# Performance work log

Hardware: AMD Instinct MI355X
Metric: run time of the kernel (lower is better)

Reference implementation:

```python
import jax, jax.numpy as jnp
import numpy as np

K = 256  # top-k causal instances (init kwarg k)


def setup_inputs() -> dict:
    key = jax.random.key(0)
    k1, k2 = jax.random.split(key)
    B, N, D = 8, 4096, 128
    X = jax.random.normal(k1, (B, N, D), dtype=jnp.float32)
    W = jax.random.normal(k2, (1, D), dtype=jnp.float32) * (1.0 / np.sqrt(D))
    return {"X": X, "W": W}


def reference(X, W):
    B, N, D = X.shape
    # --- build_adjacency_matrix, batched over B ---
    Xc = X - X.mean(axis=1, keepdims=True)                       # center per feature
    cov = jnp.einsum('bnd,bmd->bnm', Xc, Xc)                     # [B,N,N]
    var = jnp.sqrt(jnp.sum(Xc * Xc, axis=-1, keepdims=True)) + 1e-6  # [B,N,1]
    A = jnp.abs(cov / (var * var.transpose(0, 2, 1)))            # |corr|, [B,N,N]
    d = jnp.sum(A, axis=-1) ** -0.5                              # [B,N]
    A_norm = d[:, :, None] * A * d[:, None, :]                   # D^{-1/2} A D^{-1/2}
    # --- GCN layer: A_norm @ (X @ W^T), squeeze to scores ---
    S = jnp.einsum('bnm,bm->bn', A_norm, (X @ W.T)[..., 0])      # [B,N]
    # --- topk split (torch.topk is sorted descending, as is lax.top_k) ---
    _, topk_idx = jax.lax.top_k(S, K)                            # [B,K]
    mask = jnp.ones((B, N), bool).at[jnp.arange(B)[:, None], topk_idx].set(False)
    # stable argsort of ~mask puts non-topk indices first, in ascending order
    non_idx = jnp.argsort(~mask, axis=1)[:, : N - K]             # [B,N-K]
    F_c = jnp.take_along_axis(X, topk_idx[:, :, None], axis=1)   # [B,K,D]
    F_nc = jnp.take_along_axis(X, non_idx[:, :, None], axis=1)   # [B,N-K,D]
    # NOTE: original code returns F_c (not the indices) as second output (bug preserved)
    return (S, F_c, F_c.mean(axis=1, keepdims=True), F_nc.mean(axis=1, keepdims=True))
```

## Files before the change

kernel.cpp:

```cpp
#include <hip/hip_runtime.h>


#define NN 4096
#define DD 128
#define KK 256
#define KT 128
#define NBLK 128
#define LDX 132

__device__ __forceinline__ float f4c(float4 v, int c) {
  return c == 0 ? v.x : c == 1 ? v.y : c == 2 ? v.z : v.w;
}

__global__ __launch_bounds__(128) void k_mean(
    const float* __restrict__ X, float* __restrict__ mean) {
#pragma clang fp contract(off)
  int b = blockIdx.x, d = threadIdx.x;
  const float* p = X + (size_t)b * NN * DD + d;
  float acc = 0.f;
#pragma unroll 32
  for (int n = 0; n < NN; ++n) acc = acc + p[(size_t)n * DD];
  mean[b * DD + d] = acc * (1.0f / 4096.0f);
}

__global__ __launch_bounds__(256) void k_rows(
    const float* __restrict__ X, const float* __restrict__ W,
    const float* __restrict__ mean, float* __restrict__ Xc,
    float* __restrict__ vvec, float* __restrict__ yvec) {
#pragma clang fp contract(off)
  __shared__ float wL[DD], mL[DD];
  int t = threadIdx.x;
  int b = blockIdx.x >> 4;
  if (t < DD) { wL[t] = W[t]; mL[t] = mean[b * DD + t]; }
  __syncthreads();
  int rg = blockIdx.x * 256 + t;
  const float* xp = X + (size_t)rg * DD;
  float* xcp = Xc + (size_t)rg * DD;
  float xc[DD];
  float x[DD];
#pragma unroll
  for (int i = 0; i < 32; ++i) {
    float4 v4 = *(const float4*)(xp + i * 4);
    x[i*4] = v4.x; x[i*4+1] = v4.y; x[i*4+2] = v4.z; x[i*4+3] = v4.w;
  }
#pragma unroll
  for (int d = 0; d < DD; ++d) xc[d] = x[d] - mL[d];
#pragma unroll
  for (int i = 0; i < 32; ++i) {
    float4 v4; v4.x = xc[i*4]; v4.y = xc[i*4+1]; v4.z = xc[i*4+2]; v4.w = xc[i*4+3];
    *(float4*)(xcp + i * 4) = v4;
  }
  float vs = 0.f;
#pragma unroll
  for (int d = 0; d < DD; ++d) {
    float p = xc[d] * xc[d];
    vs = vs + p;
  }
  vvec[rg] = sqrtf(vs) + 1e-6f;
  float ay[8] = {0.f,0.f,0.f,0.f,0.f,0.f,0.f,0.f};
#pragma unroll
  for (int d = 0; d < DD; ++d)
    ay[d & 7] = __builtin_fmaf(x[d], wL[d], ay[d & 7]);
  float e0 = ay[0] + ay[4], e1 = ay[1] + ay[5];
  float e2 = ay[2] + ay[6], e3 = ay[3] + ay[7];
  yvec[rg] = (e0 + e2) + (e1 + e3);
}

#define GRAM_PHASE(CUR, NXT, d0v, ncv, rbv)                                  \
  {                                                                          \
    const int nc_ = (ncv);                                                   \
    _Pragma("unroll")                                                        \
    for (int q = 0; q < 2; ++q)                                              \
      _Pragma("unroll")                                                      \
      for (int c = 0; c < 4; ++c)                                            \
        NXT[q][c] = *(const float4*)(xcrow[q] + nc_ * 16 + c * 4);           \
    const int d0_ = (d0v);                                                   \
    const int rb_ = (rbv);                                                   \
    _Pragma("unroll")                                                        \
    for (int k = 0; k < 8; ++k) {                                            \
      float4 m0 = *(const float4*)&Xm[rb_ + k * 8][d0_];                     \
      float4 m1 = *(const float4*)&Xm[rb_ + k * 8][d0_ + 4];                 \
      float4 m2 = *(const float4*)&Xm[rb_ + k * 8][d0_ + 8];                 \
      float4 m3 = *(const float4*)&Xm[rb_ + k * 8][d0_ + 12];                \
      _Pragma("unroll")                                                      \
      for (int dd = 0; dd < 16; ++dd) {                                      \
        float xmv = f4c(dd < 4 ? m0 : dd < 8 ? m1 : dd < 12 ? m2 : m3,       \
                        dd & 3);                                             \
        _Pragma("unroll")                                                    \
        for (int q = 0; q < 2; ++q)                                          \
          g[k][q] = __builtin_fmaf(f4c(CUR[q][dd >> 2], dd & 3), xmv,        \
                                   g[k][q]);                                 \
      }                                                                      \
    }                                                                        \
  }

template <int PASS>
__global__ __launch_bounds__(512, 1) void k_gram(
    const float* __restrict__ Xc, const float* __restrict__ vvec,
    const float* __restrict__ dvec, const float* __restrict__ yvec,
    float* __restrict__ outv) {
#pragma clang fp contract(off)
  __shared__ float Xm[KT][LDX];
  __shared__ float vmL[KT], dmL[KT], wmL[KT];
  __shared__ float red[NBLK][8];
  int bid = blockIdx.x;
  int b = bid & 7;
  int n0 = (bid >> 3) * NBLK;
  int t = threadIdx.x;
  int j = t & 7, nl = t >> 3;
  size_t base = (size_t)b * NN * DD;

  const float* xcrow[2];
  float vnq[2], dnq[2], acc[2];
#pragma unroll
  for (int q = 0; q < 2; ++q) {
    int n = n0 + nl * 2 + q;
    xcrow[q] = Xc + base + (size_t)n * DD;
    vnq[q] = vvec[b * NN + n];
    dnq[q] = (PASS == 1) ? dvec[b * NN + n] : 0.f;
    acc[q] = 0.f;
  }

  float4 xa[2][4], xb[2][4];
#pragma unroll
  for (int q = 0; q < 2; ++q)
#pragma unroll
    for (int c = 0; c < 4; ++c)
      xa[q][c] = *(const float4*)(xcrow[q] + c * 4);

  for (int mt = 0; mt < 32; ++mt) {
    __syncthreads();
#pragma unroll
    for (int i = 0; i < 8; ++i) {
      int e = t + i * 512;
      int r = e >> 5, c4 = e & 31;
      float4 v4 = *(const float4*)(Xc + base + (size_t)(mt * KT + r) * DD + c4 * 4);
      *(float4*)&Xm[r][c4 * 4] = v4;
    }
    if (t < KT) {
      vmL[t] = vvec[b * NN + mt * KT + t];
      if (PASS == 1) {
        dmL[t] = dvec[b * NN + mt * KT + t];
        wmL[t] = yvec[b * NN + mt * KT + t];
      }
    }
    __syncthreads();

    for (int kg = 0; kg < 2; ++kg) {
      float g[8][2];
#pragma unroll
      for (int k = 0; k < 8; ++k)
#pragma unroll
        for (int q = 0; q < 2; ++q) g[k][q] = 0.f;

      int rb = kg * 64 + j;
      for (int dc4 = 0; dc4 < 4; ++dc4) {
        GRAM_PHASE(xa, xb, dc4 * 32, 2 * dc4 + 1, rb);
        GRAM_PHASE(xb, xa, dc4 * 32 + 16, (2 * dc4 + 2) & 7, rb);
      }
#pragma unroll
      for (int k = 0; k < 8; ++k) {
        int r = rb + k * 8;
        float vm = vmL[r];
        if (PASS == 0) {
#pragma unroll
          for (int q = 0; q < 2; ++q) {
            float A = fabsf(g[k][q] / (vnq[q] * vm));
            acc[q] = acc[q] + A;
          }
        } else {
          float dm = dmL[r], wm = wmL[r];
#pragma unroll
          for (int q = 0; q < 2; ++q) {
            float A = fabsf(g[k][q] / (vnq[q] * vm));
            float t2 = (dnq[q] * A) * dm;
            acc[q] = __builtin_fmaf(t2, wm, acc[q]);
          }
        }
      }
    }
  }

#pragma unroll
  for (int q = 0; q < 2; ++q) red[nl * 2 + q][j] = acc[q];
  __syncthreads();
  if (t < NBLK) {
    float r0 = red[t][0], r1 = red[t][1], r2 = red[t][2], r3 = red[t][3];
    float r4 = red[t][4], r5 = red[t][5], r6 = red[t][6], r7 = red[t][7];
    float e0 = r0 + r4, e1 = r1 + r5, e2 = r2 + r6, e3 = r3 + r7;
    outv[b * NN + n0 + t] = (e0 + e2) + (e1 + e3);
  }
}

__global__ __launch_bounds__(256) void k_d(
    const float* __restrict__ rows, float* __restrict__ dvec) {
#pragma clang fp contract(off)
  int i = blockIdx.x * 256 + threadIdx.x;
  dvec[i] = 1.0f / sqrtf(rows[i]);
}

__global__ __launch_bounds__(256) void k_rank(
    const float* __restrict__ S, int* __restrict__ tkf) {
  __shared__ float sv[NN];
  int b = blockIdx.x >> 4, chunk = blockIdx.x & 15, t = threadIdx.x;
  const float* Sb = S + (size_t)b * NN;
#pragma unroll
  for (int jj = 0; jj < 16; ++jj) sv[t + jj * 256] = Sb[t + jj * 256];
  __syncthreads();
  int n = chunk * 256 + t;
  float s = sv[n];
  int cnt = 0;
  for (int m = 0; m < NN; ++m) {
    float x = sv[m];
    cnt += (x > s) || (x == s && m < n);
  }
  if (cnt < KK) tkf[b * KK + cnt] = n;
}

__global__ __launch_bounds__(256) void k_gather(
    const float* __restrict__ X, const int* __restrict__ tkf,
    float* __restrict__ Fc) {
  int wid = threadIdx.x >> 6, lane = threadIdx.x & 63;
  int rid = blockIdx.x * 4 + wid;
  int b = rid >> 8;
  int idx = tkf[rid];
  ((float2*)Fc)[(size_t)rid * 64 + lane] =
      ((const float2*)X)[((size_t)b * NN + idx) * 64 + lane];
}

__global__ __launch_bounds__(128) void k_means_out(
    const float* __restrict__ X, const int* __restrict__ tkf,
    const float* __restrict__ mean, float* __restrict__ FcMean,
    float* __restrict__ FncMean) {
  int b = blockIdx.x, d = threadIdx.x;
  double s = 0.0;
  for (int k = 0; k < KK; ++k) {
    int idx = tkf[b * KK + k];
    s += (double)X[((size_t)b * NN + idx) * DD + d];
  }
  FcMean[b * DD + d] = (float)(s * (1.0 / 256.0));
  double colsum = (double)mean[b * DD + d] * 4096.0;
  FncMean[b * DD + d] = (float)((colsum - s) * (1.0 / 3840.0));
}

extern "C" void kernel_launch(void* const* d_in, const int* in_sizes, int n_in,
                              void* d_out, int out_size, void* d_ws,
                              size_t ws_size, hipStream_t stream) {
  (void)in_sizes; (void)n_in; (void)out_size; (void)ws_size;
  const float* X = (const float*)d_in[0];
  const float* W = (const float*)d_in[1];
  float* out = (float*)d_out;
  char* ws = (char*)d_ws;

  float* mean = (float*)(ws + 0);
  float* Xc   = (float*)(ws + 4096);
  float* vv   = (float*)(ws + 4096 + 16777216);
  float* yv   = (float*)(ws + 16912384);
  float* rows = (float*)(ws + 17043456);
  float* dv   = (float*)(ws + 17174528);
  int*   tkf  = (int*)(ws + 17305600);

  float* S_out   = out;
  float* Fc      = out + 32768;
  float* FcMean  = out + 32768 + 262144;
  float* FncMean = FcMean + 1024;

  k_mean<<<8, 128, 0, stream>>>(X, mean);
  k_rows<<<128, 256, 0, stream>>>(X, W, mean, Xc, vv, yv);
  k_gram<0><<<256, 512, 0, stream>>>(Xc, vv, dv, yv, rows);
  k_d<<<128, 256, 0, stream>>>(rows, dv);
  k_gram<1><<<256, 512, 0, stream>>>(Xc, vv, dv, yv, S_out);
  k_rank<<<128, 256, 0, stream>>>(S_out, tkf);
  k_gather<<<512, 256, 0, stream>>>(X, tkf, Fc);
  k_means_out<<<8, 128, 0, stream>>>(X, tkf, mean, FcMean, FncMean);
}
```

Measured before the change: 1.405 ms.

## Materialize correlation matrix in first pass and replace second gram pass with matvec

When the workspace is large enough, the first gram pass writes the full |corr| matrix to global memory, and the score computation becomes a memory-bound matrix-vector kernel over the stored matrix instead of recomputing the Gram products. This trades a second full compute pass for roughly 512 MB of writes plus 512 MB of reads. If the workspace is too small, it falls back to the original two-pass path.

After: 1.380 ms. Within noise of the previous version (-1.8%).

```diff
diff --git a/kernel.cpp b/kernel.cpp
--- a/kernel.cpp
+++ b/kernel.cpp
@@ -94,11 +94,11 @@
     }                                                                        \
   }
 
-template <int PASS>
+template <int PASS, int STOREA>
 __global__ __launch_bounds__(512, 1) void k_gram(
     const float* __restrict__ Xc, const float* __restrict__ vvec,
     const float* __restrict__ dvec, const float* __restrict__ yvec,
-    float* __restrict__ outv) {
+    float* __restrict__ outv, float* __restrict__ Aout) {
 #pragma clang fp contract(off)
   __shared__ float Xm[KT][LDX];
   __shared__ float vmL[KT], dmL[KT], wmL[KT];
@@ -111,11 +111,13 @@
   size_t base = (size_t)b * NN * DD;
 
   const float* xcrow[2];
+  float* aptr[2];
   float vnq[2], dnq[2], acc[2];
 #pragma unroll
   for (int q = 0; q < 2; ++q) {
     int n = n0 + nl * 2 + q;
     xcrow[q] = Xc + base + (size_t)n * DD;
+    aptr[q] = Aout + ((size_t)(b * NN + n)) * NN;
     vnq[q] = vvec[b * NN + n];
     dnq[q] = (PASS == 1) ? dvec[b * NN + n] : 0.f;
     acc[q] = 0.f;
@@ -167,6 +169,7 @@
           for (int q = 0; q < 2; ++q) {
             float A = fabsf(g[k][q] / (vnq[q] * vm));
             acc[q] = acc[q] + A;
+            if (STOREA) aptr[q][mt * KT + r] = A;
           }
         } else {
           float dm = dmL[r], wm = wmL[r];
@@ -185,6 +188,46 @@
   for (int q = 0; q < 2; ++q) red[nl * 2 + q][j] = acc[q];
   __syncthreads();
   if (t < NBLK) {
+    float r0 = red[t][0], r1 = red[t][1], r2 = red[t][2], r3 = red[t][3];
+    float r4 = red[t][4], r5 = red[t][5], r6 = red[t][6], r7 = red[t][7];
+    float e0 = r0 + r4, e1 = r1 + r5, e2 = r2 + r6, e3 = r3 + r7;
+    outv[b * NN + n0 + t] = (e0 + e2) + (e1 + e3);
+  }
+}
+
+__global__ __launch_bounds__(256) void k_scoreB(
+    const float* __restrict__ A, const float* __restrict__ dvec,
+    const float* __restrict__ yvec, float* __restrict__ outv) {
+#pragma clang fp contract(off)
+  __shared__ float dmL[NN];
+  __shared__ float wmL[NN];
+  __shared__ float red[32][8];
+  int bid = blockIdx.x;
+  int b = bid & 7;
+  int n0 = (bid >> 3) * 32;
+  int t = threadIdx.x;
+  int j = t & 7, nl = t >> 3;
+#pragma unroll
+  for (int i = 0; i < 4; ++i) {
+    int e = t + i * 256;
+    ((float4*)dmL)[e] = ((const float4*)(dvec + (size_t)b * NN))[e];
+    ((float4*)wmL)[e] = ((const float4*)(yvec + (size_t)b * NN))[e];
+  }
+  __syncthreads();
+  int n = n0 + nl;
+  float dn = dmL[n0 + nl - n0 + n0] * 0.f + dvec[(size_t)b * NN + n];
+  const float* arow = A + ((size_t)(b * NN + n)) * NN;
+  float acc = 0.f;
+#pragma unroll 8
+  for (int K = 0; K < 512; ++K) {
+    int m = j + 8 * K;
+    float Av = arow[m];
+    float t2 = (dn * Av) * dmL[m];
+    acc = __builtin_fmaf(t2, wmL[m], acc);
+  }
+  red[nl][j] = acc;
+  __syncthreads();
+  if (t < 32) {
     float r0 = red[t][0], r1 = red[t][1], r2 = red[t][2], r3 = red[t][3];
     float r4 = red[t][4], r5 = red[t][5], r6 = red[t][6], r7 = red[t][7];
     float e0 = r0 + r4, e1 = r1 + r5, e2 = r2 + r6, e3 = r3 + r7;
@@ -246,7 +289,7 @@
 extern "C" void kernel_launch(void* const* d_in, const int* in_sizes, int n_in,
                               void* d_out, int out_size, void* d_ws,
                               size_t ws_size, hipStream_t stream) {
-  (void)in_sizes; (void)n_in; (void)out_size; (void)ws_size;
+  (void)in_sizes; (void)n_in; (void)out_size;
   const float* X = (const float*)d_in[0];
   const float* W = (const float*)d_in[1];
   float* out = (float*)d_out;
@@ -259,6 +302,9 @@
   float* rows = (float*)(ws + 17043456);
   float* dv   = (float*)(ws + 17174528);
   int*   tkf  = (int*)(ws + 17305600);
+  float* Amat = (float*)(ws + 17313792);
+  const size_t NEED = 17313792ull + (size_t)8 * NN * NN * 4;
+  bool bigws = ws_size >= NEED;
 
   float* S_out   = out;
   float* Fc      = out + 32768;
@@ -267,9 +313,15 @@
 
   k_mean<<<8, 128, 0, stream>>>(X, mean);
   k_rows<<<128, 256, 0, stream>>>(X, W, mean, Xc, vv, yv);
-  k_gram<0><<<256, 512, 0, stream>>>(Xc, vv, dv, yv, rows);
-  k_d<<<128, 256, 0, stream>>>(rows, dv);
-  k_gram<1><<<256, 512, 0, stream>>>(Xc, vv, dv, yv, S_out);
+  if (bigws) {
+    k_gram<0, 1><<<256, 512, 0, stream>>>(Xc, vv, dv, yv, rows, Amat);
+    k_d<<<128, 256, 0, stream>>>(rows, dv);
+    k_scoreB<<<1024, 256, 0, stream>>>(Amat, dv, yv, S_out);
+  } else {
+    k_gram<0, 0><<<256, 512, 0, stream>>>(Xc, vv, dv, yv, rows, Amat);
+    k_d<<<128, 256, 0, stream>>>(rows, dv);
+    k_gram<1, 0><<<256, 512, 0, stream>>>(Xc, vv, dv, yv, S_out, Amat);
+  }
   k_rank<<<128, 256, 0, stream>>>(S_out, tkf);
   k_gather<<<512, 256, 0, stream>>>(X, tkf, Fc);
   k_means_out<<<8, 128, 0, stream>>>(X, tkf, mean, FcMean, FncMean);
```
